# Kernel tuning notes

Measured on AMD Instinct MI355X. Metric: run time of the kernel, lower is better.

The kernel has to match this reference:

```python
import jax, jax.numpy as jnp
import numpy as np

N, T, H, D = 32, 2048, 1024, 384

def setup_inputs() -> dict:
    key = jax.random.key(0)
    k1, k2, k3, k4, k5 = jax.random.split(key, 5)
    scale_h = 1.0 / np.sqrt(H)
    scale_d = 1.0 / np.sqrt(D)
    return {
        "gru_output": jax.random.normal(k1, (N, T, H), dtype=jnp.float32),
        "condition": jax.random.normal(k2, (N, D), dtype=jnp.float32),
        "W_h": jax.random.normal(k3, (H, H), dtype=jnp.float32) * scale_h,
        "W_c": jax.random.normal(k4, (D, H), dtype=jnp.float32) * scale_d,
        "bias": jnp.zeros((H,), dtype=jnp.float32),
        "v": jax.random.normal(k5, (H,), dtype=jnp.float32) * scale_h,
    }

def reference(gru_output, condition, W_h, W_c, bias, v):
    # h_proj: (N, T, H); c_proj: (N, 1, H)
    h_proj = jnp.einsum("nth,hk->ntk", gru_output, W_h)
    c_proj = jnp.einsum("nd,dk->nk", condition, W_c)[:, None, :]
    energy = jnp.tanh(h_proj + c_proj + bias)          # (N, T, H)
    scores = jnp.einsum("ntk,k->nt", energy, v)        # (N, T)
    weights = jax.nn.softmax(scores, axis=-1)          # (N, T)
    context = jnp.einsum("nth,nt->nh", gru_output, weights)  # (N, H)
    return context
```

## Files before the change

kernel.cpp:

```cpp
#include <hip/hip_runtime.h>
#include <hip/hip_bf16.h>

#define N_B 32
#define T_S 2048
#define H_D 1024
#define D_C 384
#define NT  (N_B * T_S)

typedef __attribute__((ext_vector_type(8))) short bf16x8;
typedef __attribute__((ext_vector_type(4))) float f32x4;

__device__ __forceinline__ ushort f2bf(float f) {
    union { float f; unsigned u; } x; x.f = f;
    unsigned u = x.u;
    unsigned r = (u + 0x7FFFu + ((u >> 16) & 1u)) >> 16;
    return (ushort)r;
}

__device__ __forceinline__ float bf2f(ushort u) {
    union { unsigned u; float f; } x; x.u = ((unsigned)u) << 16;
    return x.f;
}

__device__ __forceinline__ float fast_tanh(float x) {
    float e = __expf(2.0f * x);
    return 1.0f - 2.0f / (e + 1.0f);
}

__device__ __forceinline__ void gl2lds16(const void* g, void* l) {
    __builtin_amdgcn_global_load_lds(
        (const __attribute__((address_space(1))) void*)g,
        (__attribute__((address_space(3))) void*)l, 16, 0, 0);
}

__global__ __launch_bounds__(256) void convert_kernel(
    const float* __restrict__ g, ushort* __restrict__ gb)
{
    const size_t base = ((size_t)blockIdx.x * 256 + threadIdx.x) * 4;
    float4 v = *(const float4*)(g + base);
    ushort4 o;
    o.x = f2bf(v.x); o.y = f2bf(v.y); o.z = f2bf(v.z); o.w = f2bf(v.w);
    *(ushort4*)(gb + base) = o;
}

__global__ __launch_bounds__(256) void transpose_kernel(
    const float* __restrict__ W, ushort* __restrict__ Wt)
{
    __shared__ ushort tile[64 * 66];
    const int bx = blockIdx.x & 15;
    const int by = blockIdx.x >> 4;
    const int t = threadIdx.x;
    #pragma unroll
    for (int i = 0; i < 16; ++i) {
        int idx = t + i * 256;
        int r = idx >> 6, c = idx & 63;
        tile[r * 66 + c] = f2bf(W[(size_t)(by * 64 + r) * H_D + bx * 64 + c]);
    }
    __syncthreads();
    #pragma unroll
    for (int i = 0; i < 16; ++i) {
        int idx = t + i * 256;
        int r = idx >> 6, c = idx & 63;
        Wt[(size_t)(bx * 64 + r) * H_D + by * 64 + c] = tile[c * 66 + r];
    }
}

__global__ __launch_bounds__(256) void cproj_kernel(
    const float* __restrict__ cond, const float* __restrict__ Wc,
    const float* __restrict__ bias, float* __restrict__ cproj)
{
    const int idx = blockIdx.x * 256 + threadIdx.x;
    const int n = idx >> 10, k = idx & 1023;
    const int d0 = blockIdx.y * 96;
    float a0 = (blockIdx.y == 0) ? bias[k] : 0.f;
    float a1 = 0.f, a2 = 0.f, a3 = 0.f;
    const float* cp = cond + n * D_C;
    for (int d = d0; d < d0 + 96; d += 4) {
        a0 = fmaf(cp[d + 0], Wc[(size_t)(d + 0) * H_D + k], a0);
        a1 = fmaf(cp[d + 1], Wc[(size_t)(d + 1) * H_D + k], a1);
        a2 = fmaf(cp[d + 2], Wc[(size_t)(d + 2) * H_D + k], a2);
        a3 = fmaf(cp[d + 3], Wc[(size_t)(d + 3) * H_D + k], a3);
    }
    atomicAdd(&cproj[idx], (a0 + a1) + (a2 + a3));
}

#define BKq 32
#define TILE_U (256 * BKq)

__global__ __launch_bounds__(512, 2) void gemm4_kernel(
    const ushort* __restrict__ Ab, const ushort* __restrict__ Wt,
    const float* __restrict__ cproj, const float* __restrict__ v,
    float* __restrict__ spart)
{
    __shared__ __align__(16) ushort As[4][TILE_U];
    __shared__ __align__(16) ushort Bs[4][TILE_U];
    __shared__ float red[2][4][128];

    const int bid = blockIdx.x;
    const int wg  = (bid & 7) * 128 + (bid >> 3);
    const int mb  = wg >> 2;
    const int nb  = wg & 3;
    const int m0  = mb * 256;
    const int n0  = nb * 256;
    const int nbatch = mb >> 3;

    const int t = threadIdx.x;
    const int lane = t & 63;
    const int w = t >> 6;
    const int wm = w >> 2, wn = w & 3;
    const int ln = lane & 15, q = lane >> 4;
    const int csw = q ^ ((ln >> 1) & 3);

    const int slab = w * 2;
    const int Rl = lane >> 2;
    const int gsw = ((lane & 3) ^ ((lane >> 3) & 3)) * 8;

    const ushort* aS0 = Ab + (size_t)(m0 + slab * 16 + Rl) * H_D + gsw;
    const ushort* aS1 = aS0 + (size_t)16 * H_D;
    const ushort* bS0 = Wt + (size_t)(n0 + slab * 16 + Rl) * H_D + gsw;
    const ushort* bS1 = bS0 + (size_t)16 * H_D;
    ushort* aD = (ushort*)As + slab * 512;
    ushort* bD = (ushort*)Bs + slab * 512;

    const ushort* aR = (const ushort*)As + (wm * 128 + ln) * BKq + csw * 8;
    const ushort* bR = (const ushort*)Bs + (wn * 64  + ln) * BKq + csw * 8;

    f32x4 acc[8][4];
    #pragma unroll
    for (int i = 0; i < 8; ++i)
        #pragma unroll
        for (int j = 0; j < 4; ++j)
            acc[i][j] = (f32x4){0.f, 0.f, 0.f, 0.f};

#define ISSUE_A(kt, WB) do { const int _o = (kt) * BKq; \
    gl2lds16(aS0 + _o, aD + (WB) * TILE_U); \
    gl2lds16(aS1 + _o, aD + (WB) * TILE_U + 512); } while (0)
#define ISSUE_B(kt, WB) do { const int _o = (kt) * BKq; \
    gl2lds16(bS0 + _o, bD + (WB) * TILE_U); \
    gl2lds16(bS1 + _o, bD + (WB) * TILE_U + 512); } while (0)

#define MF(i,j,A,B) acc[i][j] = __builtin_amdgcn_mfma_f32_16x16x32_bf16(A, B, acc[i][j], 0, 0, 0)

#define TILE(kt, RB, WB, WAIT, DOISS) do { \
    asm volatile("s_waitcnt " WAIT ::: "memory"); \
    __builtin_amdgcn_s_barrier(); \
    __builtin_amdgcn_sched_barrier(0); \
    const ushort* _ar = aR + (RB) * TILE_U; \
    const ushort* _br = bR + (RB) * TILE_U; \
    bf16x8 _b0 = *(const bf16x8*)(_br); \
    bf16x8 _b1 = *(const bf16x8*)(_br + 512); \
    bf16x8 _b2 = *(const bf16x8*)(_br + 1024); \
    bf16x8 _b3 = *(const bf16x8*)(_br + 1536); \
    bf16x8 _a0 = *(const bf16x8*)(_ar); \
    bf16x8 _a1 = *(const bf16x8*)(_ar + 512); \
    bf16x8 _a2 = *(const bf16x8*)(_ar + 1024); \
    bf16x8 _a3 = *(const bf16x8*)(_ar + 1536); \
    if (DOISS) ISSUE_A((kt) + 3, WB); \
    __builtin_amdgcn_s_setprio(1); \
    MF(0,0,_a0,_b0); MF(0,1,_a0,_b1); MF(0,2,_a0,_b2); MF(0,3,_a0,_b3); \
    MF(1,0,_a1,_b0); MF(1,1,_a1,_b1); MF(1,2,_a1,_b2); MF(1,3,_a1,_b3); \
    MF(2,0,_a2,_b0); MF(2,1,_a2,_b1); MF(2,2,_a2,_b2); MF(2,3,_a2,_b3); \
    MF(3,0,_a3,_b0); MF(3,1,_a3,_b1); MF(3,2,_a3,_b2); MF(3,3,_a3,_b3); \
    __builtin_amdgcn_s_setprio(0); \
    bf16x8 _a4 = *(const bf16x8*)(_ar + 2048); \
    bf16x8 _a5 = *(const bf16x8*)(_ar + 2560); \
    bf16x8 _a6 = *(const bf16x8*)(_ar + 3072); \
    bf16x8 _a7 = *(const bf16x8*)(_ar + 3584); \
    if (DOISS) ISSUE_B((kt) + 3, WB); \
    __builtin_amdgcn_s_setprio(1); \
    MF(4,0,_a4,_b0); MF(4,1,_a4,_b1); MF(4,2,_a4,_b2); MF(4,3,_a4,_b3); \
    MF(5,0,_a5,_b0); MF(5,1,_a5,_b1); MF(5,2,_a5,_b2); MF(5,3,_a5,_b3); \
    MF(6,0,_a6,_b0); MF(6,1,_a6,_b1); MF(6,2,_a6,_b2); MF(6,3,_a6,_b3); \
    MF(7,0,_a7,_b0); MF(7,1,_a7,_b1); MF(7,2,_a7,_b2); MF(7,3,_a7,_b3); \
    __builtin_amdgcn_s_setprio(0); \
} while (0)

    ISSUE_A(0, 0); ISSUE_B(0, 0);
    ISSUE_A(1, 1); ISSUE_B(1, 1);
    ISSUE_A(2, 2); ISSUE_B(2, 2);

    #pragma unroll 1
    for (int kt = 0; kt < 28; kt += 4) {
        TILE(kt + 0, 0, 3, "vmcnt(8) lgkmcnt(0)", true);
        TILE(kt + 1, 1, 0, "vmcnt(8) lgkmcnt(0)", true);
        TILE(kt + 2, 2, 1, "vmcnt(8) lgkmcnt(0)", true);
        TILE(kt + 3, 3, 2, "vmcnt(8) lgkmcnt(0)", true);
    }
    TILE(28, 0, 3, "vmcnt(8) lgkmcnt(0)", true);
    TILE(29, 1, 0, "vmcnt(8) lgkmcnt(0)", false);
    TILE(30, 2, 0, "vmcnt(4) lgkmcnt(0)", false);
    TILE(31, 3, 0, "vmcnt(0) lgkmcnt(0)", false);

    float cpv[4], vv[4];
    {
        const float* cpn = cproj + (size_t)nbatch * H_D;
        #pragma unroll
        for (int j = 0; j < 4; ++j) {
            int col = n0 + wn * 64 + j * 16 + ln;
            cpv[j] = cpn[col];
            vv[j]  = v[col];
        }
    }
    #pragma unroll
    for (int i = 0; i < 8; ++i) {
        float s0 = 0.f, s1 = 0.f, s2 = 0.f, s3 = 0.f;
        #pragma unroll
        for (int j = 0; j < 4; ++j) {
            s0 += fast_tanh(acc[i][j][0] + cpv[j]) * vv[j];
            s1 += fast_tanh(acc[i][j][1] + cpv[j]) * vv[j];
            s2 += fast_tanh(acc[i][j][2] + cpv[j]) * vv[j];
            s3 += fast_tanh(acc[i][j][3] + cpv[j]) * vv[j];
        }
        #pragma unroll
        for (int off = 1; off < 16; off <<= 1) {
            s0 += __shfl_xor(s0, off);
            s1 += __shfl_xor(s1, off);
            s2 += __shfl_xor(s2, off);
            s3 += __shfl_xor(s3, off);
        }
        if (ln == 0) {
            red[wm][wn][i * 16 + q * 4 + 0] = s0;
            red[wm][wn][i * 16 + q * 4 + 1] = s1;
            red[wm][wn][i * 16 + q * 4 + 2] = s2;
            red[wm][wn][i * 16 + q * 4 + 3] = s3;
        }
    }
    __syncthreads();
    if (t < 256) {
        const int wm2 = t >> 7, row = t & 127;
        float val = red[wm2][0][row] + red[wm2][1][row]
                  + red[wm2][2][row] + red[wm2][3][row];
        spart[(size_t)nb * NT + m0 + wm2 * 128 + row] = val;
    }
}

__global__ __launch_bounds__(1024) void softmax8_kernel(
    const float* __restrict__ spart, float* __restrict__ weights)
{
    const int n = blockIdx.x;
    const int t = threadIdx.x;
    __shared__ float red[1024];
    float s0 = 0.f, s1 = 0.f;
    #pragma unroll
    for (int kb = 0; kb < 4; ++kb) {
        s0 += spart[(size_t)kb * NT + n * T_S + t];
        s1 += spart[(size_t)kb * NT + n * T_S + 1024 + t];
    }
    red[t] = fmaxf(s0, s1); __syncthreads();
    for (int s = 512; s > 0; s >>= 1) {
        if (t < s) red[t] = fmaxf(red[t], red[t + s]);
        __syncthreads();
    }
    const float mx = red[0];
    __syncthreads();
    float e0 = __expf(s0 - mx), e1 = __expf(s1 - mx);
    red[t] = e0 + e1; __syncthreads();
    for (int s = 512; s > 0; s >>= 1) {
        if (t < s) red[t] += red[t + s];
        __syncthreads();
    }
    const float inv = 1.0f / red[0];
    weights[n * T_S + t] = e0 * inv;
    weights[n * T_S + 1024 + t] = e1 * inv;
}

__global__ __launch_bounds__(256) void context3_kernel(
    const ushort* __restrict__ Ab, const float* __restrict__ weights,
    float* __restrict__ cpart)
{
    const int tb = blockIdx.x;
    const int n  = blockIdx.y;
    const int t  = threadIdx.x;
    float a0 = 0.f, a1 = 0.f, a2 = 0.f, a3 = 0.f;
    const float* wp = weights + n * T_S + tb * 128;
    const ushort* gp = Ab + (size_t)(n * T_S + tb * 128) * H_D + t * 4;
    #pragma unroll 8
    for (int tt = 0; tt < 128; ++tt) {
        float w = wp[tt];
        ushort4 gv = *(const ushort4*)(gp + (size_t)tt * H_D);
        a0 = fmaf(w, bf2f(gv.x), a0);
        a1 = fmaf(w, bf2f(gv.y), a1);
        a2 = fmaf(w, bf2f(gv.z), a2);
        a3 = fmaf(w, bf2f(gv.w), a3);
    }
    *(float4*)(cpart + ((size_t)tb * N_B + n) * H_D + t * 4) =
        make_float4(a0, a1, a2, a3);
}

__global__ __launch_bounds__(256) void reduce_kernel(
    const float* __restrict__ cpart, float* __restrict__ out)
{
    const int idx = blockIdx.x * 256 + threadIdx.x;
    float s = 0.f;
    #pragma unroll
    for (int tb = 0; tb < 16; ++tb)
        s += cpart[(size_t)tb * (N_B * H_D) + idx];
    out[idx] = s;
}

extern "C" void kernel_launch(void* const* d_in, const int* in_sizes, int n_in,
                              void* d_out, int out_size, void* d_ws, size_t ws_size,
                              hipStream_t stream)
{
    const float* gru  = (const float*)d_in[0];
    const float* cond = (const float*)d_in[1];
    const float* W_h  = (const float*)d_in[2];
    const float* W_c  = (const float*)d_in[3];
    const float* bias = (const float*)d_in[4];
    const float* v    = (const float*)d_in[5];
    float* out = (float*)d_out;

    char* ws = (char*)d_ws;
    const size_t szAb    = (size_t)NT * H_D * 2;
    const size_t szWt    = (size_t)H_D * H_D * 2;
    const size_t szCproj = (size_t)N_B * H_D * 4;
    const size_t szSpart = (size_t)8 * NT * 4;

    ushort* Ab    = (ushort*)ws;
    ushort* Wt    = (ushort*)(ws + szAb);
    float* cproj  = (float*)(ws + szAb + szWt);
    float* spart  = (float*)(ws + szAb + szWt + szCproj);
    float* cpart  = spart;
    float* wts    = (float*)(ws + szAb + szWt + szCproj + szSpart);

    hipMemsetAsync(cproj, 0, szCproj, stream);
    convert_kernel<<<65536, 256, 0, stream>>>(gru, Ab);
    transpose_kernel<<<256, 256, 0, stream>>>(W_h, Wt);
    cproj_kernel<<<dim3(128, 4), 256, 0, stream>>>(cond, W_c, bias, cproj);
    gemm4_kernel<<<1024, 512, 0, stream>>>(Ab, Wt, cproj, v, spart);
    softmax8_kernel<<<N_B, 1024, 0, stream>>>(spart, wts);
    context3_kernel<<<dim3(16, N_B), 256, 0, stream>>>(Ab, wts, cpart);
    reduce_kernel<<<128, 256, 0, stream>>>(cpart, out);
}
```

Baseline: 576.5 us.

## Replace direct global-to-LDS 4-stage pipeline with register-staged double buffering

The GEMM main loop no longer uses global_load_lds with a 4-deep LDS ring. Each thread now loads its tile slice into registers one step ahead, writes it to one of two LDS buffers, and computes from the other, with one barrier per k-step. LDS use is halved, which could improve occupancy. In exchange it adds VGPR pressure and explicit LDS writes, and the prefetch distance is shorter than before.

```diff
diff --git a/kernel.cpp b/kernel.cpp
--- a/kernel.cpp
+++ b/kernel.cpp
@@ -25,12 +25,6 @@
 __device__ __forceinline__ float fast_tanh(float x) {
     float e = __expf(2.0f * x);
     return 1.0f - 2.0f / (e + 1.0f);
-}
-
-__device__ __forceinline__ void gl2lds16(const void* g, void* l) {
-    __builtin_amdgcn_global_load_lds(
-        (const __attribute__((address_space(1))) void*)g,
-        (__attribute__((address_space(3))) void*)l, 16, 0, 0);
 }
 
 __global__ __launch_bounds__(256) void convert_kernel(
@@ -87,13 +81,13 @@
 #define BKq 32
 #define TILE_U (256 * BKq)
 
-__global__ __launch_bounds__(512, 2) void gemm4_kernel(
+__global__ __launch_bounds__(512, 2) void gemm5_kernel(
     const ushort* __restrict__ Ab, const ushort* __restrict__ Wt,
     const float* __restrict__ cproj, const float* __restrict__ v,
     float* __restrict__ spart)
 {
-    __shared__ __align__(16) ushort As[4][TILE_U];
-    __shared__ __align__(16) ushort Bs[4][TILE_U];
+    __shared__ __align__(16) ushort As[2][TILE_U];
+    __shared__ __align__(16) ushort Bs[2][TILE_U];
     __shared__ float red[2][4][128];
 
     const int bid = blockIdx.x;
@@ -111,16 +105,18 @@
     const int ln = lane & 15, q = lane >> 4;
     const int csw = q ^ ((ln >> 1) & 3);
 
-    const int slab = w * 2;
-    const int Rl = lane >> 2;
-    const int gsw = ((lane & 3) ^ ((lane >> 3) & 3)) * 8;
-
-    const ushort* aS0 = Ab + (size_t)(m0 + slab * 16 + Rl) * H_D + gsw;
-    const ushort* aS1 = aS0 + (size_t)16 * H_D;
-    const ushort* bS0 = Wt + (size_t)(n0 + slab * 16 + Rl) * H_D + gsw;
-    const ushort* bS1 = bS0 + (size_t)16 * H_D;
-    ushort* aD = (ushort*)As + slab * 512;
-    ushort* bD = (ushort*)Bs + slab * 512;
+    const int srow = t >> 1;
+    const int c0   = (t & 1) * 2;
+    const int fsw  = (srow >> 1) & 3;
+    const int wc0  = (c0 ^ fsw) * 8;
+    const int wc1  = ((c0 + 1) ^ fsw) * 8;
+
+    const ushort* aL = Ab + (size_t)(m0 + srow) * H_D + c0 * 8;
+    const ushort* bL = Wt + (size_t)(n0 + srow) * H_D + c0 * 8;
+    ushort* awp0 = (ushort*)As + srow * BKq + wc0;
+    ushort* awp1 = (ushort*)As + srow * BKq + wc1;
+    ushort* bwp0 = (ushort*)Bs + srow * BKq + wc0;
+    ushort* bwp1 = (ushort*)Bs + srow * BKq + wc1;
 
     const ushort* aR = (const ushort*)As + (wm * 128 + ln) * BKq + csw * 8;
     const ushort* bR = (const ushort*)Bs + (wn * 64  + ln) * BKq + csw * 8;
@@ -132,19 +128,25 @@
         for (int j = 0; j < 4; ++j)
             acc[i][j] = (f32x4){0.f, 0.f, 0.f, 0.f};
 
-#define ISSUE_A(kt, WB) do { const int _o = (kt) * BKq; \
-    gl2lds16(aS0 + _o, aD + (WB) * TILE_U); \
-    gl2lds16(aS1 + _o, aD + (WB) * TILE_U + 512); } while (0)
-#define ISSUE_B(kt, WB) do { const int _o = (kt) * BKq; \
-    gl2lds16(bS0 + _o, bD + (WB) * TILE_U); \
-    gl2lds16(bS1 + _o, bD + (WB) * TILE_U + 512); } while (0)
+    bf16x8 sA0, sA1, sB0, sB1;
+
+#define LOADS(kt) do { \
+    const ushort* _a = aL + (kt) * BKq; \
+    const ushort* _b = bL + (kt) * BKq; \
+    sA0 = *(const bf16x8*)(_a);     sA1 = *(const bf16x8*)(_a + 8); \
+    sB0 = *(const bf16x8*)(_b);     sB1 = *(const bf16x8*)(_b + 8); \
+} while (0)
+
+#define WRITES(buf) do { \
+    *(bf16x8*)(awp0 + (buf) * TILE_U) = sA0; \
+    *(bf16x8*)(awp1 + (buf) * TILE_U) = sA1; \
+    *(bf16x8*)(bwp0 + (buf) * TILE_U) = sB0; \
+    *(bf16x8*)(bwp1 + (buf) * TILE_U) = sB1; \
+} while (0)
 
 #define MF(i,j,A,B) acc[i][j] = __builtin_amdgcn_mfma_f32_16x16x32_bf16(A, B, acc[i][j], 0, 0, 0)
 
-#define TILE(kt, RB, WB, WAIT, DOISS) do { \
-    asm volatile("s_waitcnt " WAIT ::: "memory"); \
-    __builtin_amdgcn_s_barrier(); \
-    __builtin_amdgcn_sched_barrier(0); \
+#define COMPUTE(RB) do { \
     const ushort* _ar = aR + (RB) * TILE_U; \
     const ushort* _br = bR + (RB) * TILE_U; \
     bf16x8 _b0 = *(const bf16x8*)(_br); \
@@ -155,7 +157,6 @@
     bf16x8 _a1 = *(const bf16x8*)(_ar + 512); \
     bf16x8 _a2 = *(const bf16x8*)(_ar + 1024); \
     bf16x8 _a3 = *(const bf16x8*)(_ar + 1536); \
-    if (DOISS) ISSUE_A((kt) + 3, WB); \
     __builtin_amdgcn_s_setprio(1); \
     MF(0,0,_a0,_b0); MF(0,1,_a0,_b1); MF(0,2,_a0,_b2); MF(0,3,_a0,_b3); \
     MF(1,0,_a1,_b0); MF(1,1,_a1,_b1); MF(1,2,_a1,_b2); MF(1,3,_a1,_b3); \
@@ -166,7 +167,6 @@
     bf16x8 _a5 = *(const bf16x8*)(_ar + 2560); \
     bf16x8 _a6 = *(const bf16x8*)(_ar + 3072); \
     bf16x8 _a7 = *(const bf16x8*)(_ar + 3584); \
-    if (DOISS) ISSUE_B((kt) + 3, WB); \
     __builtin_amdgcn_s_setprio(1); \
     MF(4,0,_a4,_b0); MF(4,1,_a4,_b1); MF(4,2,_a4,_b2); MF(4,3,_a4,_b3); \
     MF(5,0,_a5,_b0); MF(5,1,_a5,_b1); MF(5,2,_a5,_b2); MF(5,3,_a5,_b3); \
@@ -175,21 +175,24 @@
     __builtin_amdgcn_s_setprio(0); \
 } while (0)
 
-    ISSUE_A(0, 0); ISSUE_B(0, 0);
-    ISSUE_A(1, 1); ISSUE_B(1, 1);
-    ISSUE_A(2, 2); ISSUE_B(2, 2);
+#define FENCE do { \
+    asm volatile("s_waitcnt lgkmcnt(0)" ::: "memory"); \
+    __builtin_amdgcn_s_barrier(); \
+    __builtin_amdgcn_sched_barrier(0); \
+} while (0)
+
+    LOADS(0);
+    WRITES(0);
+    LOADS(1);
+    FENCE;
 
     #pragma unroll 1
-    for (int kt = 0; kt < 28; kt += 4) {
-        TILE(kt + 0, 0, 3, "vmcnt(8) lgkmcnt(0)", true);
-        TILE(kt + 1, 1, 0, "vmcnt(8) lgkmcnt(0)", true);
-        TILE(kt + 2, 2, 1, "vmcnt(8) lgkmcnt(0)", true);
-        TILE(kt + 3, 3, 2, "vmcnt(8) lgkmcnt(0)", true);
-    }
-    TILE(28, 0, 3, "vmcnt(8) lgkmcnt(0)", true);
-    TILE(29, 1, 0, "vmcnt(8) lgkmcnt(0)", false);
-    TILE(30, 2, 0, "vmcnt(4) lgkmcnt(0)", false);
-    TILE(31, 3, 0, "vmcnt(0) lgkmcnt(0)", false);
+    for (int kt = 0; kt < 30; kt += 2) {
+        WRITES(1); LOADS(kt + 2); COMPUTE(0); FENCE;
+        WRITES(0); LOADS(kt + 3); COMPUTE(1); FENCE;
+    }
+    WRITES(1); COMPUTE(0); FENCE;
+    COMPUTE(1);
 
     float cpv[4], vv[4];
     {
@@ -327,7 +330,7 @@
     convert_kernel<<<65536, 256, 0, stream>>>(gru, Ab);
     transpose_kernel<<<256, 256, 0, stream>>>(W_h, Wt);
     cproj_kernel<<<dim3(128, 4), 256, 0, stream>>>(cond, W_c, bias, cproj);
-    gemm4_kernel<<<1024, 512, 0, stream>>>(Ab, Wt, cproj, v, spart);
+    gemm5_kernel<<<1024, 512, 0, stream>>>(Ab, Wt, cproj, v, spart);
     softmax8_kernel<<<N_B, 1024, 0, stream>>>(spart, wts);
     context3_kernel<<<dim3(16, N_B), 256, 0, stream>>>(Ab, wts, cpart);
     reduce_kernel<<<128, 256, 0, stream>>>(cpart, out);
```

New measurement: 571.5 us. About the same (-0.9%).

## Rework GEMM to 3-stage LDS pipeline and grid-stride the conversion kernel

Applied to the files above, without the earlier changes.

The GEMM pipeline moves from four LDS buffers with a prefetch distance of three to three buffers with a prefetch distance of two. Each wave now stages contiguous 16-row slabs split into two 128-row halves, and the B read base is remapped to match. Global-to-LDS loads are now issued right after the barrier, with explicit lgkmcnt waits before each MFMA group. This cuts LDS use per block, which may help occupancy, but leaves less latency hiding. The fp32-to-bf16 conversion kernel now launches 2048 blocks, each looping over 32 strided chunks, instead of 65536 one-shot blocks, to reduce block launch overhead.

```diff
diff --git a/kernel.cpp b/kernel.cpp
--- a/kernel.cpp
+++ b/kernel.cpp
@@ -36,11 +36,16 @@
 __global__ __launch_bounds__(256) void convert_kernel(
     const float* __restrict__ g, ushort* __restrict__ gb)
 {
-    const size_t base = ((size_t)blockIdx.x * 256 + threadIdx.x) * 4;
-    float4 v = *(const float4*)(g + base);
-    ushort4 o;
-    o.x = f2bf(v.x); o.y = f2bf(v.y); o.z = f2bf(v.z); o.w = f2bf(v.w);
-    *(ushort4*)(gb + base) = o;
+    const size_t g0 = ((size_t)blockIdx.x * 256 + threadIdx.x) * 4;
+    const size_t stride = (size_t)2048 * 256 * 4;
+    #pragma unroll 4
+    for (int i = 0; i < 32; ++i) {
+        const size_t base = g0 + (size_t)i * stride;
+        float4 v = *(const float4*)(g + base);
+        ushort4 o;
+        o.x = f2bf(v.x); o.y = f2bf(v.y); o.z = f2bf(v.z); o.w = f2bf(v.w);
+        *(ushort4*)(gb + base) = o;
+    }
 }
 
 __global__ __launch_bounds__(256) void transpose_kernel(
@@ -84,16 +89,15 @@
     atomicAdd(&cproj[idx], (a0 + a1) + (a2 + a3));
 }
 
-#define BKq 32
-#define TILE_U (256 * BKq)
-
-__global__ __launch_bounds__(512, 2) void gemm4_kernel(
+#define BK7 32
+
+__global__ __launch_bounds__(512, 2) void gemm7_kernel(
     const ushort* __restrict__ Ab, const ushort* __restrict__ Wt,
     const float* __restrict__ cproj, const float* __restrict__ v,
     float* __restrict__ spart)
 {
-    __shared__ __align__(16) ushort As[4][TILE_U];
-    __shared__ __align__(16) ushort Bs[4][TILE_U];
+    __shared__ __align__(16) ushort As[3][2][4096];
+    __shared__ __align__(16) ushort Bs[3][2][4096];
     __shared__ float red[2][4][128];
 
     const int bid = blockIdx.x;
@@ -108,22 +112,17 @@
     const int lane = t & 63;
     const int w = t >> 6;
     const int wm = w >> 2, wn = w & 3;
+    const int wh = wn >> 1;
     const int ln = lane & 15, q = lane >> 4;
-    const int csw = q ^ ((ln >> 1) & 3);
-
-    const int slab = w * 2;
-    const int Rl = lane >> 2;
-    const int gsw = ((lane & 3) ^ ((lane >> 3) & 3)) * 8;
-
-    const ushort* aS0 = Ab + (size_t)(m0 + slab * 16 + Rl) * H_D + gsw;
-    const ushort* aS1 = aS0 + (size_t)16 * H_D;
-    const ushort* bS0 = Wt + (size_t)(n0 + slab * 16 + Rl) * H_D + gsw;
-    const ushort* bS1 = bS0 + (size_t)16 * H_D;
-    ushort* aD = (ushort*)As + slab * 512;
-    ushort* bD = (ushort*)Bs + slab * 512;
-
-    const ushort* aR = (const ushort*)As + (wm * 128 + ln) * BKq + csw * 8;
-    const ushort* bR = (const ushort*)Bs + (wn * 64  + ln) * BKq + csw * 8;
+    const int rsw = (q ^ ((ln >> 1) & 3)) * 8;
+
+    const int rr   = w * 16 + (lane >> 2);
+    const int clog = (lane & 3) ^ ((lane >> 3) & 3);
+    const ushort* aSrc = Ab + (size_t)(m0 + rr) * H_D + clog * 8;
+    const ushort* bSrc = Wt + (size_t)(n0 + rr) * H_D + clog * 8;
+
+    const ushort* aRbase = &As[0][0][0] + wm * 4096 + ln * 32 + rsw;
+    const ushort* bRbase = &Bs[0][0][0] + wh * 4096 + (wn & 1) * 2048 + ln * 32 + rsw;
 
     f32x4 acc[8][4];
     #pragma unroll
@@ -132,21 +131,22 @@
         for (int j = 0; j < 4; ++j)
             acc[i][j] = (f32x4){0.f, 0.f, 0.f, 0.f};
 
-#define ISSUE_A(kt, WB) do { const int _o = (kt) * BKq; \
-    gl2lds16(aS0 + _o, aD + (WB) * TILE_U); \
-    gl2lds16(aS1 + _o, aD + (WB) * TILE_U + 512); } while (0)
-#define ISSUE_B(kt, WB) do { const int _o = (kt) * BKq; \
-    gl2lds16(bS0 + _o, bD + (WB) * TILE_U); \
-    gl2lds16(bS1 + _o, bD + (WB) * TILE_U + 512); } while (0)
+#define STAGE_A(kt2, buf, half) \
+    gl2lds16(aSrc + (size_t)(half) * 128 * H_D + (kt2) * BK7, \
+             (ushort*)&As[0][0][0] + (buf) * 8192 + (half) * 4096 + w * 512)
+#define STAGE_B(kt2, buf, half) \
+    gl2lds16(bSrc + (size_t)(half) * 128 * H_D + (kt2) * BK7, \
+             (ushort*)&Bs[0][0][0] + (buf) * 8192 + (half) * 4096 + w * 512)
 
 #define MF(i,j,A,B) acc[i][j] = __builtin_amdgcn_mfma_f32_16x16x32_bf16(A, B, acc[i][j], 0, 0, 0)
 
-#define TILE(kt, RB, WB, WAIT, DOISS) do { \
+#define TILE(kt, B0, B2, WAIT) do { \
     asm volatile("s_waitcnt " WAIT ::: "memory"); \
     __builtin_amdgcn_s_barrier(); \
     __builtin_amdgcn_sched_barrier(0); \
-    const ushort* _ar = aR + (RB) * TILE_U; \
-    const ushort* _br = bR + (RB) * TILE_U; \
+    if ((kt) + 2 < 32) { STAGE_A((kt) + 2, B2, 0); STAGE_A((kt) + 2, B2, 1); } \
+    const ushort* _ar = aRbase + (B0) * 8192; \
+    const ushort* _br = bRbase + (B0) * 8192; \
     bf16x8 _b0 = *(const bf16x8*)(_br); \
     bf16x8 _b1 = *(const bf16x8*)(_br + 512); \
     bf16x8 _b2 = *(const bf16x8*)(_br + 1024); \
@@ -155,18 +155,21 @@
     bf16x8 _a1 = *(const bf16x8*)(_ar + 512); \
     bf16x8 _a2 = *(const bf16x8*)(_ar + 1024); \
     bf16x8 _a3 = *(const bf16x8*)(_ar + 1536); \
-    if (DOISS) ISSUE_A((kt) + 3, WB); \
+    asm volatile("s_waitcnt lgkmcnt(0)" ::: "memory"); \
+    __builtin_amdgcn_sched_barrier(0); \
     __builtin_amdgcn_s_setprio(1); \
     MF(0,0,_a0,_b0); MF(0,1,_a0,_b1); MF(0,2,_a0,_b2); MF(0,3,_a0,_b3); \
     MF(1,0,_a1,_b0); MF(1,1,_a1,_b1); MF(1,2,_a1,_b2); MF(1,3,_a1,_b3); \
     MF(2,0,_a2,_b0); MF(2,1,_a2,_b1); MF(2,2,_a2,_b2); MF(2,3,_a2,_b3); \
     MF(3,0,_a3,_b0); MF(3,1,_a3,_b1); MF(3,2,_a3,_b2); MF(3,3,_a3,_b3); \
     __builtin_amdgcn_s_setprio(0); \
+    if ((kt) + 2 < 32) { STAGE_B((kt) + 2, B2, 0); STAGE_B((kt) + 2, B2, 1); } \
     bf16x8 _a4 = *(const bf16x8*)(_ar + 2048); \
     bf16x8 _a5 = *(const bf16x8*)(_ar + 2560); \
     bf16x8 _a6 = *(const bf16x8*)(_ar + 3072); \
     bf16x8 _a7 = *(const bf16x8*)(_ar + 3584); \
-    if (DOISS) ISSUE_B((kt) + 3, WB); \
+    asm volatile("s_waitcnt lgkmcnt(0)" ::: "memory"); \
+    __builtin_amdgcn_sched_barrier(0); \
     __builtin_amdgcn_s_setprio(1); \
     MF(4,0,_a4,_b0); MF(4,1,_a4,_b1); MF(4,2,_a4,_b2); MF(4,3,_a4,_b3); \
     MF(5,0,_a5,_b0); MF(5,1,_a5,_b1); MF(5,2,_a5,_b2); MF(5,3,_a5,_b3); \
@@ -175,21 +178,17 @@
     __builtin_amdgcn_s_setprio(0); \
 } while (0)
 
-    ISSUE_A(0, 0); ISSUE_B(0, 0);
-    ISSUE_A(1, 1); ISSUE_B(1, 1);
-    ISSUE_A(2, 2); ISSUE_B(2, 2);
+    STAGE_A(0, 0, 0); STAGE_A(0, 0, 1); STAGE_B(0, 0, 0); STAGE_B(0, 0, 1);
+    STAGE_A(1, 1, 0); STAGE_A(1, 1, 1); STAGE_B(1, 1, 0); STAGE_B(1, 1, 1);
 
     #pragma unroll 1
-    for (int kt = 0; kt < 28; kt += 4) {
-        TILE(kt + 0, 0, 3, "vmcnt(8) lgkmcnt(0)", true);
-        TILE(kt + 1, 1, 0, "vmcnt(8) lgkmcnt(0)", true);
-        TILE(kt + 2, 2, 1, "vmcnt(8) lgkmcnt(0)", true);
-        TILE(kt + 3, 3, 2, "vmcnt(8) lgkmcnt(0)", true);
-    }
-    TILE(28, 0, 3, "vmcnt(8) lgkmcnt(0)", true);
-    TILE(29, 1, 0, "vmcnt(8) lgkmcnt(0)", false);
-    TILE(30, 2, 0, "vmcnt(4) lgkmcnt(0)", false);
-    TILE(31, 3, 0, "vmcnt(0) lgkmcnt(0)", false);
+    for (int kt = 0; kt < 30; kt += 3) {
+        TILE(kt + 0, 0, 2, "vmcnt(4)");
+        TILE(kt + 1, 1, 0, "vmcnt(4)");
+        TILE(kt + 2, 2, 1, "vmcnt(4)");
+    }
+    TILE(30, 0, 2, "vmcnt(4)");
+    TILE(31, 1, 0, "vmcnt(0)");
 
     float cpv[4], vv[4];
     {
@@ -324,10 +323,10 @@
     float* wts    = (float*)(ws + szAb + szWt + szCproj + szSpart);
 
     hipMemsetAsync(cproj, 0, szCproj, stream);
-    convert_kernel<<<65536, 256, 0, stream>>>(gru, Ab);
+    convert_kernel<<<2048, 256, 0, stream>>>(gru, Ab);
     transpose_kernel<<<256, 256, 0, stream>>>(W_h, Wt);
     cproj_kernel<<<dim3(128, 4), 256, 0, stream>>>(cond, W_c, bias, cproj);
-    gemm4_kernel<<<1024, 512, 0, stream>>>(Ab, Wt, cproj, v, spart);
+    gemm7_kernel<<<1024, 512, 0, stream>>>(Ab, Wt, cproj, v, spart);
     softmax8_kernel<<<N_B, 1024, 0, stream>>>(spart, wts);
     context3_kernel<<<dim3(16, N_B), 256, 0, stream>>>(Ab, wts, cpart);
     reduce_kernel<<<128, 256, 0, stream>>>(cpart, out);
```

Result: no change. 582.7 us (+1.1%).
